# Kernel tuning notes

Measured on AMD Instinct MI355X. Metric: run time of the kernel, lower is better.

Reference implementation:

```python
import jax, jax.numpy as jnp
import numpy as np

N = 50000   # nodes
E = 400000  # edges
G = 256     # graphs in batch
D = 256     # out_dim (scalar channel width)
VD = 16     # vector channel width after v_emb


def setup_inputs() -> dict:
    key = jax.random.key(0)
    ks = jax.random.split(key, 12)

    def rn(k, shape, scale=0.02):
        return (jax.random.normal(k, shape) * scale).astype(jnp.float32)

    return dict(
        node_s=jax.random.normal(ks[0], (N, 23), jnp.float32),
        node_v=jax.random.normal(ks[1], (N, 4, 3), jnp.float32),
        edge_s=jax.random.normal(ks[2], (E, 17), jnp.float32),
        edge_index=jax.random.randint(ks[3], (2, E), 0, N, jnp.int32),
        batch=jnp.sort(jax.random.randint(ks[4], (N,), 0, G, jnp.int32)),
        Ws=rn(ks[5], (23, D)), bs=jnp.zeros((D,), jnp.float32),
        Wv=rn(ks[6], (4, VD)), bv=jnp.zeros((VD,), jnp.float32),
        We=rn(ks[7], (18, D)), be=jnp.zeros((D,), jnp.float32),
        Wm1=rn(ks[8], (2 * D + VD + D, D)), bm1=jnp.zeros((D,), jnp.float32),
        Wm2=rn(ks[9], (D, D)), bm2=jnp.zeros((D,), jnp.float32),
        Wn=rn(ks[10], (D + VD, D)), bn=jnp.zeros((D,), jnp.float32),
        gamma=jnp.ones((D,), jnp.float32), beta=jnp.zeros((D,), jnp.float32),
    )


def reference(node_s, node_v, edge_s, edge_index, batch,
              Ws, bs, Wv, bv, We, be, Wm1, bm1, Wm2, bm2, Wn, bn, gamma, beta):
    # --- embeddings ---
    s = node_s @ Ws + bs                                            # [N, D]
    e_in = jnp.concatenate([edge_s, jnp.zeros((edge_s.shape[0], 1), edge_s.dtype)], axis=-1)  # no edge_v branch
    e = e_in @ We + be                                              # [E, D]
    # v_emb: Linear over the 4 vector channels -> [N, VD, 3]
    v = jnp.einsum('nkc,ko->noc', node_v, Wv) + bv[None, :, None]
    v_norm = jnp.linalg.norm(v, axis=-1)                            # [N, VD]

    # --- SimpleGVPConv: gather -> 2-layer MLP per edge -> scatter-mean ---
    src, dst = edge_index[0], edge_index[1]                         # PyG: s_j = s[src], s_i = s[dst]
    m_in = jnp.concatenate([s[dst], s[src], v_norm[src], e], axis=-1)  # [E, 2D+VD+D]
    m = jax.nn.relu(m_in @ Wm1 + bm1) @ Wm2 + bm2                   # [E, D]
    agg = jax.ops.segment_sum(m, dst, num_segments=N)               # [N, D]
    cnt = jax.ops.segment_sum(jnp.ones((E,), m.dtype), dst, num_segments=N)
    s = s + agg / jnp.maximum(cnt, 1.0)[:, None]                    # mean aggr + residual update

    # --- node MLP: Linear -> LayerNorm -> ReLU (dropout = eval identity) ---
    feat = jnp.concatenate([s, v_norm], axis=-1)                    # [N, D+VD]
    h = feat @ Wn + bn                                              # [N, D]
    mu = h.mean(axis=-1, keepdims=True)
    var = h.var(axis=-1, keepdims=True)
    h = (h - mu) * jax.lax.rsqrt(var + 1e-5) * gamma + beta
    h = jax.nn.relu(h)

    # --- global mean pool ---
    gsum = jax.ops.segment_sum(h, batch, num_segments=G)            # [G, D]
    gcnt = jax.ops.segment_sum(jnp.ones((h.shape[0],), h.dtype), batch, num_segments=G)
    return gsum / jnp.maximum(gcnt, 1.0)[:, None]
```

## Files before the change

kernel.cpp:

```cpp
#include <hip/hip_runtime.h>
#include <hip/hip_bf16.h>

typedef unsigned short u16;
typedef __attribute__((ext_vector_type(8))) short short8;
typedef __attribute__((ext_vector_type(4))) short short4v;
typedef __attribute__((ext_vector_type(4))) float f32x4;

#define NN 50000
#define EE 400000
#define GG 256
#define MP 50048
#define KS 64
#define K2 320
#define EWS 260

static __device__ __forceinline__ __hip_bfloat16 f2b(float x) { return __float2bfloat16(x); }
static __device__ __forceinline__ float u16tof(u16 v) {
    unsigned x = ((unsigned)v) << 16;
    float f;
    __builtin_memcpy(&f, &x, 4);
    return f;
}
static __device__ __forceinline__ u16 ftou16(float x) {
    __hip_bfloat16 h = __float2bfloat16(x);
    u16 b;
    __builtin_memcpy(&b, &h, 2);
    return b;
}

static __device__ __forceinline__ float dot256(const float* __restrict__ a,
                                               const float* __restrict__ b, int c) {
    const float* __restrict__ bp = b + c;
    float s0 = 0.f, s1 = 0.f, s2 = 0.f, s3 = 0.f;
    float s4 = 0.f, s5 = 0.f, s6 = 0.f, s7 = 0.f;
#pragma unroll 4
    for (int j = 0; j < 256; j += 8) {
        s0 += a[j]     * bp[(size_t)(j)     * 256];
        s1 += a[j + 1] * bp[(size_t)(j + 1) * 256];
        s2 += a[j + 2] * bp[(size_t)(j + 2) * 256];
        s3 += a[j + 3] * bp[(size_t)(j + 3) * 256];
        s4 += a[j + 4] * bp[(size_t)(j + 4) * 256];
        s5 += a[j + 5] * bp[(size_t)(j + 5) * 256];
        s6 += a[j + 6] * bp[(size_t)(j + 6) * 256];
        s7 += a[j + 7] * bp[(size_t)(j + 7) * 256];
    }
    return ((s0 + s1) + (s2 + s3)) + ((s4 + s5) + (s6 + s7));
}

__global__ __launch_bounds__(256) void phase1(const float* __restrict__ Wm1,
                                              const float* __restrict__ Wn,
                                              const float* __restrict__ Wm2,
                                              const float* __restrict__ We,
                                              const float* __restrict__ be,
                                              const float* __restrict__ bm1,
                                              const float* __restrict__ bm2,
                                              const float* __restrict__ Ws,
                                              const float* __restrict__ bs,
                                              __hip_bfloat16* __restrict__ W1pqT,
                                              __hip_bfloat16* __restrict__ W2T,
                                              float* __restrict__ Wc, float* __restrict__ bc,
                                              float* __restrict__ crow,
                                              const float* __restrict__ node_s,
                                              const float* __restrict__ node_v,
                                              const float* __restrict__ Wv,
                                              const float* __restrict__ bv,
                                              __hip_bfloat16* __restrict__ XL2,
                                              const int* __restrict__ ei,
                                              const int* __restrict__ batch,
                                              int* __restrict__ cnt,
                                              int* __restrict__ gstart) {
    int blk = blockIdx.x, tid = threadIdx.x;
    if (blk < 64) {
        int k = blk;
#pragma unroll
        for (int half = 0; half < 2; ++half) {
            int c = half * 256 + tid;
            int cc = c & 255;
            const float* Wm1h = (c < 256) ? Wm1 : (Wm1 + 256 * 256);
            float v = 0.f;
            if (k < 23) v = dot256(&Ws[k * 256], Wm1h, cc);
            else if (k < 39) { if (c >= 256) v = Wm1[(512 + (k - 23)) * 256 + cc]; }
            else if (k == 39) v = dot256(bs, Wm1h, cc);
            W1pqT[c * KS + k] = f2b(v);
        }
    } else if (blk < 74) {
        int wb = blk - 64;
        int kt0 = (wb >> 1) * 64;
        int c0 = (wb & 1) * 128;
        int w = tid >> 6, lane = tid & 63;
        int quad = lane >> 4, l16 = lane & 15;
        f32x4 acc[4][2] = {};
        for (int jt = 0; jt < 256; jt += 32) {
            int j0 = jt + quad * 8;
            short8 af[4], bf[2];
#pragma unroll
            for (int mi = 0; mi < 4; ++mi) {
                int k = kt0 + mi * 16 + l16;
                const float* ar = nullptr;
                if (k < 23) ar = Ws + (size_t)k * 256;
                else if (k == 39) ar = bs;
                else if (k >= 40 && k < 296) ar = Wm2 + (size_t)(k - 40) * 256;
                float v0 = 0.f, v1 = 0.f, v2 = 0.f, v3 = 0.f, v4 = 0.f, v5 = 0.f, v6 = 0.f, v7 = 0.f;
                if (ar) {
                    f32x4 x0 = *(const f32x4*)(ar + j0);
                    f32x4 x1 = *(const f32x4*)(ar + j0 + 4);
                    v0 = x0[0]; v1 = x0[1]; v2 = x0[2]; v3 = x0[3];
                    v4 = x1[0]; v5 = x1[1]; v6 = x1[2]; v7 = x1[3];
                }
                af[mi][0] = (short)ftou16(v0); af[mi][1] = (short)ftou16(v1);
                af[mi][2] = (short)ftou16(v2); af[mi][3] = (short)ftou16(v3);
                af[mi][4] = (short)ftou16(v4); af[mi][5] = (short)ftou16(v5);
                af[mi][6] = (short)ftou16(v6); af[mi][7] = (short)ftou16(v7);
            }
#pragma unroll
            for (int ni = 0; ni < 2; ++ni) {
                int c = c0 + w * 32 + ni * 16 + l16;
#pragma unroll
                for (int u = 0; u < 8; ++u)
                    bf[ni][u] = (short)ftou16(Wn[(size_t)(j0 + u) * 256 + c]);
            }
#pragma unroll
            for (int mi = 0; mi < 4; ++mi) {
#pragma unroll
                for (int ni = 0; ni < 2; ++ni)
                    acc[mi][ni] = __builtin_amdgcn_mfma_f32_16x16x32_bf16(af[mi], bf[ni], acc[mi][ni], 0, 0, 0);
            }
        }
#pragma unroll
        for (int mi = 0; mi < 4; ++mi) {
#pragma unroll
            for (int ni = 0; ni < 2; ++ni) {
                int c = c0 + w * 32 + ni * 16 + l16;
#pragma unroll
                for (int r = 0; r < 4; ++r) {
                    int k = kt0 + mi * 16 + quad * 4 + r;
                    float v = acc[mi][ni][r];
                    if (k >= 23 && k < 39) v = Wn[(size_t)(256 + k - 23) * 256 + c];
                    W2T[(size_t)c * K2 + k] = f2b(v);
                }
            }
        }
    } else if (blk < 93) {
        int b = blk - 74, c = tid;
        if (b < 17) Wc[b * 256 + c] = dot256(&We[b * 256], &Wm1[528 * 256], c);
        else if (b == 17) bc[c] = bm1[c] + dot256(be, &Wm1[528 * 256], c);
        else crow[c] = dot256(bm2, Wn, c);
    } else if (blk < 12593) {
        int w = tid >> 6, lane = tid & 63;
        int n = (blk - 93) * 4 + w;
        if (n < NN) {
            float lv = (lane < 23) ? node_s[(size_t)n * 23 + lane] : 0.f;
            float vv = (lane < 12) ? node_v[(size_t)n * 12 + lane] : 0.f;
            float nvk[12];
#pragma unroll
            for (int k = 0; k < 12; ++k) nvk[k] = __shfl(vv, k, 64);
            float vn = 0.f;
            if (lane < 16) {
                float b0 = bv[lane];
                float vx = b0, vy = b0, vz = b0;
#pragma unroll
                for (int k = 0; k < 4; ++k) {
                    float wv = Wv[k * 16 + lane];
                    vx += nvk[k * 3 + 0] * wv;
                    vy += nvk[k * 3 + 1] * wv;
                    vz += nvk[k * 3 + 2] * wv;
                }
                vn = sqrtf(vx * vx + vy * vy + vz * vz);
            }
            int vsrc = (lane >= 23 && lane < 39) ? (lane - 23) : 0;
            float vbc = __shfl(vn, vsrc, 64);
            float outv;
            if (lane < 23) outv = lv;
            else if (lane < 39) outv = vbc;
            else if (lane == 39) outv = 1.f;
            else outv = 0.f;
            __hip_bfloat16* row = XL2 + (size_t)n * K2;
            row[lane] = f2b(outv);
            if (lane < 24) row[296 + lane] = f2b(0.f);
        }
    } else if (blk < 14156) {
        int e = (blk - 12593) * 256 + tid;
        if (e < EE) atomicAdd(&cnt[ei[EE + e]], 1);
    } else {
        int n = (blk - 14156) * 256 + tid;
        if (n < NN) {
            int bn = batch[n];
            int bp = (n == 0) ? -1 : batch[n - 1];
            for (int g = bp + 1; g <= bn; ++g) gstart[g] = n;
            if (n == NN - 1)
                for (int g = bn + 1; g <= GG; ++g) gstart[g] = NN;
        }
    }
}

__global__ __launch_bounds__(256) void scan1(const int* __restrict__ cnt, int* __restrict__ rowptr,
                                             int* __restrict__ bsum) {
    int tid = threadIdx.x, i = blockIdx.x * 256 + tid;
    __shared__ int sd[256];
    int v = (i < NN) ? cnt[i] : 0;
    sd[tid] = v;
    __syncthreads();
    for (int off = 1; off < 256; off <<= 1) {
        int t = (tid >= off) ? sd[tid - off] : 0;
        __syncthreads();
        sd[tid] += t;
        __syncthreads();
    }
    if (i < NN) rowptr[i] = sd[tid] - v;
    if (tid == 255) bsum[blockIdx.x] = sd[255];
}
__global__ __launch_bounds__(256) void scan2(int* __restrict__ bsum, const int* __restrict__ gstart,
                                             float* __restrict__ ginv) {
    int c = threadIdx.x;
    __shared__ int sd[256];
    int v = (c < 196) ? bsum[c] : 0;
    sd[c] = v;
    __syncthreads();
    for (int off = 1; off < 256; off <<= 1) {
        int t = (c >= off) ? sd[c - off] : 0;
        __syncthreads();
        sd[c] += t;
        __syncthreads();
    }
    if (c < 196) bsum[c] = sd[c] - v;
    ginv[c] = 1.f / fmaxf((float)(gstart[c + 1] - gstart[c]), 1.f);
}
__global__ __launch_bounds__(256) void scan3(const int* __restrict__ cnt, const int* __restrict__ bsum,
                                             int* __restrict__ rowptr, int* __restrict__ cursor) {
    int i = blockIdx.x * 256 + threadIdx.x;
    if (i < NN) {
        int v = rowptr[i] + bsum[blockIdx.x];
        rowptr[i] = v;
        cursor[i] = v;
        if (i == NN - 1) rowptr[NN] = v + cnt[i];
    }
}

__global__ __launch_bounds__(256, 2) void gemm1_fill(const u16* __restrict__ A, const u16* __restrict__ Bt,
                                                     __hip_bfloat16* __restrict__ C,
                                                     const int* __restrict__ ei, int* __restrict__ cursor,
                                                     int* __restrict__ eid, int* __restrict__ srcv,
                                                     const float* __restrict__ Wc,
                                                     u16* __restrict__ WcBf) {
    __shared__ __align__(16) u16 At[128 * 64];
    __shared__ __align__(16) u16 Bs[128 * 64];
    int blk = blockIdx.x, tid = threadIdx.x;
    if (blk >= 1564) {
        if (blk == 3127) {
            for (int idx = tid; idx < 8192; idx += 256) {
                int ni = idx >> 9;
                int l = (idx >> 3) & 63;
                int j = idx & 7;
                int k = ((l >> 4) << 3) + j;
                int c = ni * 16 + (l & 15);
                float v = (k < 17) ? Wc[k * 256 + c] : 0.f;
                WcBf[idx] = ftou16(v);
            }
            return;
        }
        int e = (blk - 1564) * 256 + tid;
        if (e < EE) {
            int d = ei[EE + e];
            int s = ei[e];
            int pos = atomicAdd(&cursor[d], 1);
            eid[pos] = e;
            srcv[pos] = s;
        }
        return;
    }
    long m0 = (long)(blk >> 2) * 128;
    long n0 = (long)(blk & 3) * 128;
    int wid = tid >> 6, lane = tid & 63;
    int wm = wid >> 1, wn = wid & 1;
    int quad = lane >> 4, l16 = lane & 15;
    f32x4 acc[4][4] = {};
    int r0 = tid >> 3;
    int cc = (tid & 7) * 8;
    const u16* Ab = A + (m0 + r0) * K2 + cc;
    const u16* Bb = Bt + (n0 + r0) * KS + cc;
#pragma unroll
    for (int i = 0; i < 4; ++i) {
        int row = r0 + i * 32;
        __builtin_amdgcn_global_load_lds(
            (const __attribute__((address_space(1))) void*)(Ab + (long)(i * 32) * K2),
            (__attribute__((address_space(3))) void*)(&At[row * 64 + cc]), 16, 0, 0);
    }
#pragma unroll
    for (int i = 0; i < 4; ++i) {
        int row = r0 + i * 32;
        __builtin_amdgcn_global_load_lds(
            (const __attribute__((address_space(1))) void*)(Bb + (long)(i * 32) * KS),
            (__attribute__((address_space(3))) void*)(&Bs[row * 64 + cc]), 16, 0, 0);
    }
    __syncthreads();
#pragma unroll
    for (int kk = 0; kk < 64; kk += 32) {
        short8 af[4], bf[4];
#pragma unroll
        for (int mi = 0; mi < 4; ++mi)
            af[mi] = *(const short8*)&At[(wm * 64 + mi * 16 + l16) * 64 + kk + quad * 8];
#pragma unroll
        for (int ni = 0; ni < 4; ++ni)
            bf[ni] = *(const short8*)&Bs[(wn * 64 + ni * 16 + l16) * 64 + kk + quad * 8];
#pragma unroll
        for (int mi = 0; mi < 4; ++mi) {
#pragma unroll
            for (int ni = 0; ni < 4; ++ni)
                acc[mi][ni] = __builtin_amdgcn_mfma_f32_16x16x32_bf16(af[mi], bf[ni], acc[mi][ni], 0, 0, 0);
        }
    }
#pragma unroll
    for (int mi = 0; mi < 4; ++mi) {
#pragma unroll
        for (int ni = 0; ni < 4; ++ni) {
            long row = m0 + wm * 64 + mi * 16 + quad * 4;
            long col = n0 + wn * 64 + ni * 16 + l16;
#pragma unroll
            for (int r = 0; r < 4; ++r)
                C[(row + r) * 512 + col] = f2b(acc[mi][ni][r]);
        }
    }
}

__global__ __launch_bounds__(64) void edge_agg(const u16* __restrict__ PQ,
                                               const float* __restrict__ edge_s,
                                               const int* __restrict__ srcv,
                                               const int* __restrict__ eid,
                                               const int* __restrict__ rowptr,
                                               const u16* __restrict__ WcBf,
                                               const float* __restrict__ bc,
                                               __hip_bfloat16* __restrict__ XL2) {
    __shared__ __align__(16) u16 EW[16 * EWS];
    int lane = threadIdx.x;
    int n = blockIdx.x;
    int start = rowptr[n], deg = rowptr[n + 1] - start;
    int l16 = lane & 15, quad = lane >> 4;
    short8 wcf[16];
#pragma unroll
    for (int ni = 0; ni < 16; ++ni)
        wcf[ni] = *(const short8*)&WcBf[ni * 512 + lane * 8];
    f32x4 bc4 = *(const f32x4*)&bc[lane * 4];
    short4v p4 = *(const short4v*)&PQ[(size_t)n * 512 + lane * 4];
    f32x4 pb;
#pragma unroll
    for (int i = 0; i < 4; ++i) pb[i] = u16tof((u16)p4[i]) + bc4[i];
    f32x4 acc = {0.f, 0.f, 0.f, 0.f};
    const f32x4 zf = {0.f, 0.f, 0.f, 0.f};
    for (int base = 0; base < deg; base += 64) {
        int m = deg - base;
        if (m > 64) m = 64;
        int mm1 = m - 1;
        int ee = 0, ss = 0;
        if (lane < m) {
            ee = eid[start + base + lane];
            ss = srcv[start + base + lane];
        }
        auto loadQ = [&](int p) {
            int pc = (p < mm1) ? p : mm1;
            int s = __builtin_amdgcn_readlane(ss, pc);
            return *(const short4v*)&PQ[(size_t)s * 512 + 256 + lane * 4];
        };
        int ng = (m + 15) >> 4;
        for (int g = 0; g < ng; ++g) {
            int b16 = g * 16;
            short4v qA0 = loadQ(b16 + 0);
            short4v qA1 = loadQ(b16 + 1);
            short4v qA2 = loadQ(b16 + 2);
            short4v qA3 = loadQ(b16 + 3);
            short4v qA4 = loadQ(b16 + 4);
            short4v qA5 = loadQ(b16 + 5);
            short4v qA6 = loadQ(b16 + 6);
            short4v qA7 = loadQ(b16 + 7);
            int li = b16 + l16;
            if (li > mm1) li = mm1;
            int ev = __shfl(ee, li, 64);
            const float* ep = edge_s + (size_t)ev * 17 + quad * 8;
            float a0 = 0.f, a1 = 0.f, a2 = 0.f, a3 = 0.f, a4 = 0.f, a5 = 0.f, a6 = 0.f, a7 = 0.f;
            if (quad < 2) {
                a0 = ep[0]; a1 = ep[1]; a2 = ep[2]; a3 = ep[3];
                a4 = ep[4]; a5 = ep[5]; a6 = ep[6]; a7 = ep[7];
            } else if (quad == 2) {
                a0 = ep[0];
            }
            short8 af;
            af[0] = (short)ftou16(a0); af[1] = (short)ftou16(a1);
            af[2] = (short)ftou16(a2); af[3] = (short)ftou16(a3);
            af[4] = (short)ftou16(a4); af[5] = (short)ftou16(a5);
            af[6] = (short)ftou16(a6); af[7] = (short)ftou16(a7);
#pragma unroll
            for (int ni = 0; ni < 16; ++ni) {
                f32x4 ew = __builtin_amdgcn_mfma_f32_16x16x32_bf16(af, wcf[ni], zf, 0, 0, 0);
#pragma unroll
                for (int r = 0; r < 4; ++r)
                    EW[(quad * 4 + r) * EWS + ni * 16 + l16] = ftou16(ew[r]);
            }
            int mg = m - b16;
            if (mg > 16) mg = 16;
            short4v qB0 = {0, 0, 0, 0}, qB1 = {0, 0, 0, 0}, qB2 = {0, 0, 0, 0}, qB3 = {0, 0, 0, 0};
            short4v qB4 = {0, 0, 0, 0}, qB5 = {0, 0, 0, 0}, qB6 = {0, 0, 0, 0}, qB7 = {0, 0, 0, 0};
            if (mg > 8) {
                qB0 = loadQ(b16 + 8);
                qB1 = loadQ(b16 + 9);
                qB2 = loadQ(b16 + 10);
                qB3 = loadQ(b16 + 11);
                qB4 = loadQ(b16 + 12);
                qB5 = loadQ(b16 + 13);
                qB6 = loadQ(b16 + 14);
                qB7 = loadQ(b16 + 15);
            }
#define CONSUME(QQ, c)                                                              \
            {                                                                       \
                int jj = (c);                                                       \
                if (jj < mg) {                                                      \
                    short4v ew4 = *(const short4v*)&EW[jj * EWS + lane * 4];        \
                    _Pragma("unroll")                                               \
                    for (int i = 0; i < 4; ++i)                                     \
                        acc[i] += fmaxf(pb[i] + u16tof((u16)QQ[i]) +                \
                                        u16tof((u16)ew4[i]), 0.f);                  \
                }                                                                   \
            }
            CONSUME(qA0, 0)  CONSUME(qA1, 1)  CONSUME(qA2, 2)  CONSUME(qA3, 3)
            CONSUME(qA4, 4)  CONSUME(qA5, 5)  CONSUME(qA6, 6)  CONSUME(qA7, 7)
            CONSUME(qB0, 8)  CONSUME(qB1, 9)  CONSUME(qB2, 10) CONSUME(qB3, 11)
            CONSUME(qB4, 12) CONSUME(qB5, 13) CONSUME(qB6, 14) CONSUME(qB7, 15)
#undef CONSUME
        }
    }
    float inv = 1.f / fmaxf((float)deg, 1.f);
    short4v ov;
#pragma unroll
    for (int i = 0; i < 4; ++i) ov[i] = (short)ftou16(acc[i] * inv);
    *(short4v*)&XL2[(size_t)n * K2 + 40 + lane * 4] = ov;
}

__global__ __launch_bounds__(256, 2) void gemm2_lnp(const u16* __restrict__ A, const u16* __restrict__ Bt,
                                                    const int* __restrict__ cnt, const int* __restrict__ batch,
                                                    const float* __restrict__ bn, const float* __restrict__ crow,
                                                    const float* __restrict__ gamma, const float* __restrict__ beta,
                                                    const float* __restrict__ ginv, float* __restrict__ out) {
    __shared__ __align__(16) u16 At[64 * 64];
    __shared__ __align__(16) u16 Bs[256 * 64];
    __shared__ float rsum[4][64], rsum2[4][64];
    __shared__ int sdeg[64], sbatch[64];
    int tid = threadIdx.x;
    long m0 = (long)blockIdx.x * 64;
    int w = tid >> 6, lane = tid & 63;
    int quad = lane >> 4, l16 = lane & 15;
    f32x4 acc[4][4] = {};
    int r0 = tid >> 3;
    int cc = (tid & 7) * 8;
    const u16* Ab = A + (m0 + r0) * K2 + cc;
    const u16* Bb = Bt + (long)r0 * K2 + cc;
    for (int kt = 0; kt < K2; kt += 64) {
#pragma unroll
        for (int i = 0; i < 2; ++i) {
            int row = r0 + i * 32;
            __builtin_amdgcn_global_load_lds(
                (const __attribute__((address_space(1))) void*)(Ab + (long)(i * 32) * K2 + kt),
                (__attribute__((address_space(3))) void*)(&At[row * 64 + cc]), 16, 0, 0);
        }
#pragma unroll
        for (int i = 0; i < 8; ++i) {
            int row = r0 + i * 32;
            __builtin_amdgcn_global_load_lds(
                (const __attribute__((address_space(1))) void*)(Bb + (long)(i * 32) * K2 + kt),
                (__attribute__((address_space(3))) void*)(&Bs[row * 64 + cc]), 16, 0, 0);
        }
        __syncthreads();
#pragma unroll
        for (int kk = 0; kk < 64; kk += 32) {
            short8 af[4], bf[4];
#pragma unroll
            for (int mi = 0; mi < 4; ++mi)
                af[mi] = *(const short8*)&At[(mi * 16 + l16) * 64 + kk + quad * 8];
#pragma unroll
            for (int ni = 0; ni < 4; ++ni)
                bf[ni] = *(const short8*)&Bs[(w * 64 + ni * 16 + l16) * 64 + kk + quad * 8];
#pragma unroll
            for (int mi = 0; mi < 4; ++mi) {
#pragma unroll
                for (int ni = 0; ni < 4; ++ni)
                    acc[mi][ni] = __builtin_amdgcn_mfma_f32_16x16x32_bf16(af[mi], bf[ni], acc[mi][ni], 0, 0, 0);
            }
        }
        __syncthreads();
    }
    if (tid < 64) {
        long n = m0 + tid;
        sdeg[tid] = (n < NN) ? cnt[n] : 0;
        sbatch[tid] = (n < NN) ? batch[n] : -1;
    }
    __syncthreads();
    float bn_l[4], cr_l[4], g_l[4], be_l[4];
#pragma unroll
    for (int ni = 0; ni < 4; ++ni) {
        int col = w * 64 + ni * 16 + l16;
        bn_l[ni] = bn[col];
        cr_l[ni] = crow[col];
        g_l[ni] = gamma[col];
        be_l[ni] = beta[col];
    }
#pragma unroll
    for (int mi = 0; mi < 4; ++mi) {
#pragma unroll
        for (int r = 0; r < 4; ++r) {
            int row = mi * 16 + quad * 4 + r;
            float cr_on = (sdeg[row] > 0) ? 1.f : 0.f;
            float s = 0.f, s2 = 0.f;
#pragma unroll
            for (int ni = 0; ni < 4; ++ni) {
                float xv = acc[mi][ni][r] + bn_l[ni] + cr_on * cr_l[ni];
                acc[mi][ni][r] = xv;
                s += xv;
                s2 += xv * xv;
            }
            s += __shfl_xor(s, 1, 64);  s2 += __shfl_xor(s2, 1, 64);
            s += __shfl_xor(s, 2, 64);  s2 += __shfl_xor(s2, 2, 64);
            s += __shfl_xor(s, 4, 64);  s2 += __shfl_xor(s2, 4, 64);
            s += __shfl_xor(s, 8, 64);  s2 += __shfl_xor(s2, 8, 64);
            if (l16 == 0) { rsum[w][row] = s; rsum2[w][row] = s2; }
        }
    }
    __syncthreads();
    float mu_a[4][4], rs_a[4][4];
#pragma unroll
    for (int mi = 0; mi < 4; ++mi) {
#pragma unroll
        for (int r = 0; r < 4; ++r) {
            int row = mi * 16 + quad * 4 + r;
            float S = rsum[0][row] + rsum[1][row] + rsum[2][row] + rsum[3][row];
            float S2 = rsum2[0][row] + rsum2[1][row] + rsum2[2][row] + rsum2[3][row];
            float mu = S * (1.f / 256.f);
            mu_a[mi][r] = mu;
            rs_a[mi][r] = rsqrtf(S2 * (1.f / 256.f) - mu * mu + 1e-5f);
        }
    }
#pragma unroll
    for (int ni = 0; ni < 4; ++ni) {
        int col = w * 64 + ni * 16 + l16;
        float pacc = 0.f;
        int curg = -1;
#pragma unroll
        for (int mi = 0; mi < 4; ++mi) {
#pragma unroll
            for (int r = 0; r < 4; ++r) {
                int row = mi * 16 + quad * 4 + r;
                int g = sbatch[row];
                float y = (acc[mi][ni][r] - mu_a[mi][r]) * rs_a[mi][r] * g_l[ni] + be_l[ni];
                y = fmaxf(y, 0.f);
                if (g != curg) {
                    if (curg >= 0) atomicAdd(&out[curg * 256 + col], pacc * ginv[curg]);
                    pacc = 0.f;
                    curg = g;
                }
                if (g >= 0) pacc += y;
            }
        }
        if (curg >= 0) atomicAdd(&out[curg * 256 + col], pacc * ginv[curg]);
    }
}

extern "C" void kernel_launch(void* const* d_in, const int* in_sizes, int n_in,
                              void* d_out, int out_size, void* d_ws, size_t ws_size,
                              hipStream_t stream) {
    const float* node_s = (const float*)d_in[0];
    const float* node_v = (const float*)d_in[1];
    const float* edge_s = (const float*)d_in[2];
    const int* ei = (const int*)d_in[3];
    const int* batch = (const int*)d_in[4];
    const float* Ws = (const float*)d_in[5];
    const float* bs = (const float*)d_in[6];
    const float* Wv = (const float*)d_in[7];
    const float* bv = (const float*)d_in[8];
    const float* We = (const float*)d_in[9];
    const float* be = (const float*)d_in[10];
    const float* Wm1 = (const float*)d_in[11];
    const float* bm1 = (const float*)d_in[12];
    const float* Wm2 = (const float*)d_in[13];
    const float* bm2 = (const float*)d_in[14];
    const float* Wn = (const float*)d_in[15];
    const float* bn = (const float*)d_in[16];
    const float* gamma = (const float*)d_in[17];
    const float* beta = (const float*)d_in[18];

    char* ws = (char*)d_ws;
    size_t off = 0;
    auto take = [&](size_t n) {
        void* p = ws + off;
        off = (off + n + 255) & ~(size_t)255;
        return p;
    };
    __hip_bfloat16* XL2 = (__hip_bfloat16*)take((size_t)MP * K2 * 2);
    __hip_bfloat16* PQ = (__hip_bfloat16*)take((size_t)MP * 512 * 2);
    __hip_bfloat16* W1pqT = (__hip_bfloat16*)take(512 * KS * 2);
    __hip_bfloat16* W2T = (__hip_bfloat16*)take(256 * K2 * 2);
    float* Wc = (float*)take(17 * 256 * 4);
    float* bc = (float*)take(256 * 4);
    float* crow = (float*)take(256 * 4);
    u16* WcBf = (u16*)take(16 * 512 * 2);
    int* cnt = (int*)take(NN * 4);
    int* gstart = (int*)take((GG + 1) * 4);
    float* ginv = (float*)take(GG * 4);
    int* rowptr = (int*)take((NN + 1) * 4);
    int* cursor = (int*)take(NN * 4);
    int* eid = (int*)take(EE * 4);
    int* srcv = (int*)take(EE * 4);
    int* bsum = (int*)take(256 * 4);

    hipMemsetAsync(cnt, 0, NN * 4, stream);
    hipMemsetAsync(d_out, 0, (size_t)out_size * 4, stream);

    phase1<<<14352, 256, 0, stream>>>(Wm1, Wn, Wm2, We, be, bm1, bm2, Ws, bs,
                                      W1pqT, W2T, Wc, bc, crow,
                                      node_s, node_v, Wv, bv, XL2, ei, batch, cnt, gstart);

    scan1<<<196, 256, 0, stream>>>(cnt, rowptr, bsum);
    scan2<<<1, 256, 0, stream>>>(bsum, gstart, ginv);
    scan3<<<196, 256, 0, stream>>>(cnt, bsum, rowptr, cursor);

    gemm1_fill<<<3128, 256, 0, stream>>>((const u16*)XL2, (const u16*)W1pqT, PQ, ei, cursor, eid,
                                         srcv, Wc, WcBf);

    edge_agg<<<NN, 64, 0, stream>>>((const u16*)PQ, edge_s, srcv, eid, rowptr, WcBf, bc, XL2);

    gemm2_lnp<<<782, 256, 0, stream>>>((const u16*)XL2, (const u16*)W2T, cnt, batch,
                                       bn, crow, gamma, beta, ginv, (float*)d_out);
}
```

Measured before the change: 291.0 us.

## Make edge_agg persistent with next-node prefetch; compute W1pq fold via MFMA

edge_agg now launches a fixed 4096 single-wave blocks that loop over nodes with stride 4096 instead of one block per node. Each block prefetches the next node's row pointers, first 64 edge/source ids and P row while it processes the current node. This amortises the per-block setup, including the 16 WcBf fragment loads, and hides index-load latency. Separately, the Ws·Wm1 fold in phase1 moves from 64 blocks of scalar dot products to 4 MFMA blocks, so fewer blocks carry more work each and load balance across nodes of different degree may suffer.

```diff
diff --git a/kernel.cpp b/kernel.cpp
--- a/kernel.cpp
+++ b/kernel.cpp
@@ -13,6 +13,7 @@
 #define KS 64
 #define K2 320
 #define EWS 260
+#define EAG 4096
 
 static __device__ __forceinline__ __hip_bfloat16 f2b(float x) { return __float2bfloat16(x); }
 static __device__ __forceinline__ float u16tof(u16 v) {
@@ -70,21 +71,65 @@
                                               int* __restrict__ cnt,
                                               int* __restrict__ gstart) {
     int blk = blockIdx.x, tid = threadIdx.x;
-    if (blk < 64) {
-        int k = blk;
-#pragma unroll
-        for (int half = 0; half < 2; ++half) {
-            int c = half * 256 + tid;
-            int cc = c & 255;
-            const float* Wm1h = (c < 256) ? Wm1 : (Wm1 + 256 * 256);
-            float v = 0.f;
-            if (k < 23) v = dot256(&Ws[k * 256], Wm1h, cc);
-            else if (k < 39) { if (c >= 256) v = Wm1[(512 + (k - 23)) * 256 + cc]; }
-            else if (k == 39) v = dot256(bs, Wm1h, cc);
-            W1pqT[c * KS + k] = f2b(v);
-        }
-    } else if (blk < 74) {
-        int wb = blk - 64;
+    if (blk < 4) {
+        int c0 = blk * 128;
+        int w = tid >> 6, lane = tid & 63;
+        int quad = lane >> 4, l16 = lane & 15;
+        f32x4 acc[4][2] = {};
+        for (int jt = 0; jt < 256; jt += 32) {
+            int j0 = jt + quad * 8;
+            short8 af[4], bf[2];
+#pragma unroll
+            for (int mi = 0; mi < 4; ++mi) {
+                int k = mi * 16 + l16;
+                const float* ar = nullptr;
+                if (k < 23) ar = Ws + (size_t)k * 256;
+                else if (k == 39) ar = bs;
+                float v0 = 0.f, v1 = 0.f, v2 = 0.f, v3 = 0.f, v4 = 0.f, v5 = 0.f, v6 = 0.f, v7 = 0.f;
+                if (ar) {
+                    f32x4 x0 = *(const f32x4*)(ar + j0);
+                    f32x4 x1 = *(const f32x4*)(ar + j0 + 4);
+                    v0 = x0[0]; v1 = x0[1]; v2 = x0[2]; v3 = x0[3];
+                    v4 = x1[0]; v5 = x1[1]; v6 = x1[2]; v7 = x1[3];
+                }
+                af[mi][0] = (short)ftou16(v0); af[mi][1] = (short)ftou16(v1);
+                af[mi][2] = (short)ftou16(v2); af[mi][3] = (short)ftou16(v3);
+                af[mi][4] = (short)ftou16(v4); af[mi][5] = (short)ftou16(v5);
+                af[mi][6] = (short)ftou16(v6); af[mi][7] = (short)ftou16(v7);
+            }
+#pragma unroll
+            for (int ni = 0; ni < 2; ++ni) {
+                int c = c0 + w * 32 + ni * 16 + l16;
+                const float* Wm1h = (c < 256) ? Wm1 : (Wm1 + 256 * 256);
+                int cc = c & 255;
+#pragma unroll
+                for (int u = 0; u < 8; ++u)
+                    bf[ni][u] = (short)ftou16(Wm1h[(size_t)(j0 + u) * 256 + cc]);
+            }
+#pragma unroll
+            for (int mi = 0; mi < 4; ++mi) {
+#pragma unroll
+                for (int ni = 0; ni < 2; ++ni)
+                    acc[mi][ni] = __builtin_amdgcn_mfma_f32_16x16x32_bf16(af[mi], bf[ni], acc[mi][ni], 0, 0, 0);
+            }
+        }
+#pragma unroll
+        for (int mi = 0; mi < 4; ++mi) {
+#pragma unroll
+            for (int ni = 0; ni < 2; ++ni) {
+                int c = c0 + w * 32 + ni * 16 + l16;
+#pragma unroll
+                for (int r = 0; r < 4; ++r) {
+                    int k = mi * 16 + quad * 4 + r;
+                    float v = acc[mi][ni][r];
+                    if (k >= 23 && k < 39)
+                        v = (c >= 256) ? Wm1[(size_t)(512 + (k - 23)) * 256 + (c & 255)] : 0.f;
+                    W1pqT[(size_t)c * KS + k] = f2b(v);
+                }
+            }
+        }
+    } else if (blk < 14) {
+        int wb = blk - 4;
         int kt0 = (wb >> 1) * 64;
         int c0 = (wb & 1) * 128;
         int w = tid >> 6, lane = tid & 63;
@@ -140,14 +185,14 @@
                 }
             }
         }
-    } else if (blk < 93) {
-        int b = blk - 74, c = tid;
+    } else if (blk < 33) {
+        int b = blk - 14, c = tid;
         if (b < 17) Wc[b * 256 + c] = dot256(&We[b * 256], &Wm1[528 * 256], c);
         else if (b == 17) bc[c] = bm1[c] + dot256(be, &Wm1[528 * 256], c);
         else crow[c] = dot256(bm2, Wn, c);
-    } else if (blk < 12593) {
+    } else if (blk < 12533) {
         int w = tid >> 6, lane = tid & 63;
-        int n = (blk - 93) * 4 + w;
+        int n = (blk - 33) * 4 + w;
         if (n < NN) {
             float lv = (lane < 23) ? node_s[(size_t)n * 23 + lane] : 0.f;
             float vv = (lane < 12) ? node_v[(size_t)n * 12 + lane] : 0.f;
@@ -178,11 +223,11 @@
             row[lane] = f2b(outv);
             if (lane < 24) row[296 + lane] = f2b(0.f);
         }
-    } else if (blk < 14156) {
-        int e = (blk - 12593) * 256 + tid;
+    } else if (blk < 14096) {
+        int e = (blk - 12533) * 256 + tid;
         if (e < EE) atomicAdd(&cnt[ei[EE + e]], 1);
     } else {
-        int n = (blk - 14156) * 256 + tid;
+        int n = (blk - 14096) * 256 + tid;
         if (n < NN) {
             int bn = batch[n];
             int bp = (n == 0) ? -1 : batch[n - 1];
@@ -332,105 +377,138 @@
                                                __hip_bfloat16* __restrict__ XL2) {
     __shared__ __align__(16) u16 EW[16 * EWS];
     int lane = threadIdx.x;
-    int n = blockIdx.x;
-    int start = rowptr[n], deg = rowptr[n + 1] - start;
     int l16 = lane & 15, quad = lane >> 4;
     short8 wcf[16];
 #pragma unroll
     for (int ni = 0; ni < 16; ++ni)
         wcf[ni] = *(const short8*)&WcBf[ni * 512 + lane * 8];
     f32x4 bc4 = *(const f32x4*)&bc[lane * 4];
+    const f32x4 zf = {0.f, 0.f, 0.f, 0.f};
+    int n = blockIdx.x;
+    int st = rowptr[n], en = rowptr[n + 1];
+    int ee = 0, ss = 0;
+    {
+        int m0 = en - st;
+        if (m0 > 64) m0 = 64;
+        if (lane < m0) {
+            ee = eid[st + lane];
+            ss = srcv[st + lane];
+        }
+    }
     short4v p4 = *(const short4v*)&PQ[(size_t)n * 512 + lane * 4];
-    f32x4 pb;
-#pragma unroll
-    for (int i = 0; i < 4; ++i) pb[i] = u16tof((u16)p4[i]) + bc4[i];
-    f32x4 acc = {0.f, 0.f, 0.f, 0.f};
-    const f32x4 zf = {0.f, 0.f, 0.f, 0.f};
-    for (int base = 0; base < deg; base += 64) {
-        int m = deg - base;
-        if (m > 64) m = 64;
-        int mm1 = m - 1;
-        int ee = 0, ss = 0;
-        if (lane < m) {
-            ee = eid[start + base + lane];
-            ss = srcv[start + base + lane];
-        }
-        auto loadQ = [&](int p) {
-            int pc = (p < mm1) ? p : mm1;
-            int s = __builtin_amdgcn_readlane(ss, pc);
-            return *(const short4v*)&PQ[(size_t)s * 512 + 256 + lane * 4];
-        };
-        int ng = (m + 15) >> 4;
-        for (int g = 0; g < ng; ++g) {
-            int b16 = g * 16;
-            short4v qA0 = loadQ(b16 + 0);
-            short4v qA1 = loadQ(b16 + 1);
-            short4v qA2 = loadQ(b16 + 2);
-            short4v qA3 = loadQ(b16 + 3);
-            short4v qA4 = loadQ(b16 + 4);
-            short4v qA5 = loadQ(b16 + 5);
-            short4v qA6 = loadQ(b16 + 6);
-            short4v qA7 = loadQ(b16 + 7);
-            int li = b16 + l16;
-            if (li > mm1) li = mm1;
-            int ev = __shfl(ee, li, 64);
-            const float* ep = edge_s + (size_t)ev * 17 + quad * 8;
-            float a0 = 0.f, a1 = 0.f, a2 = 0.f, a3 = 0.f, a4 = 0.f, a5 = 0.f, a6 = 0.f, a7 = 0.f;
-            if (quad < 2) {
-                a0 = ep[0]; a1 = ep[1]; a2 = ep[2]; a3 = ep[3];
-                a4 = ep[4]; a5 = ep[5]; a6 = ep[6]; a7 = ep[7];
-            } else if (quad == 2) {
-                a0 = ep[0];
-            }
-            short8 af;
-            af[0] = (short)ftou16(a0); af[1] = (short)ftou16(a1);
-            af[2] = (short)ftou16(a2); af[3] = (short)ftou16(a3);
-            af[4] = (short)ftou16(a4); af[5] = (short)ftou16(a5);
-            af[6] = (short)ftou16(a6); af[7] = (short)ftou16(a7);
-#pragma unroll
-            for (int ni = 0; ni < 16; ++ni) {
-                f32x4 ew = __builtin_amdgcn_mfma_f32_16x16x32_bf16(af, wcf[ni], zf, 0, 0, 0);
-#pragma unroll
-                for (int r = 0; r < 4; ++r)
-                    EW[(quad * 4 + r) * EWS + ni * 16 + l16] = ftou16(ew[r]);
-            }
-            int mg = m - b16;
-            if (mg > 16) mg = 16;
-            short4v qB0 = {0, 0, 0, 0}, qB1 = {0, 0, 0, 0}, qB2 = {0, 0, 0, 0}, qB3 = {0, 0, 0, 0};
-            short4v qB4 = {0, 0, 0, 0}, qB5 = {0, 0, 0, 0}, qB6 = {0, 0, 0, 0}, qB7 = {0, 0, 0, 0};
-            if (mg > 8) {
-                qB0 = loadQ(b16 + 8);
-                qB1 = loadQ(b16 + 9);
-                qB2 = loadQ(b16 + 10);
-                qB3 = loadQ(b16 + 11);
-                qB4 = loadQ(b16 + 12);
-                qB5 = loadQ(b16 + 13);
-                qB6 = loadQ(b16 + 14);
-                qB7 = loadQ(b16 + 15);
-            }
+    while (true) {
+        int nn = n + EAG;
+        int stN = 0, enN = 0, eeN = 0, ssN = 0;
+        short4v p4N = {0, 0, 0, 0};
+        if (nn < NN) {
+            stN = rowptr[nn];
+            enN = rowptr[nn + 1];
+            int mN = enN - stN;
+            if (mN > 64) mN = 64;
+            if (lane < mN) {
+                eeN = eid[stN + lane];
+                ssN = srcv[stN + lane];
+            }
+            p4N = *(const short4v*)&PQ[(size_t)nn * 512 + lane * 4];
+        }
+        int deg = en - st;
+        f32x4 pb;
+#pragma unroll
+        for (int i = 0; i < 4; ++i) pb[i] = u16tof((u16)p4[i]) + bc4[i];
+        f32x4 acc = {0.f, 0.f, 0.f, 0.f};
+        for (int base = 0; base < deg; base += 64) {
+            int m = deg - base;
+            if (m > 64) m = 64;
+            int mm1 = m - 1;
+            if (base > 0) {
+                ee = 0; ss = 0;
+                if (lane < m) {
+                    ee = eid[st + base + lane];
+                    ss = srcv[st + base + lane];
+                }
+            }
+            auto loadQ = [&](int p) {
+                int pc = (p < mm1) ? p : mm1;
+                int s = __builtin_amdgcn_readlane(ss, pc);
+                return *(const short4v*)&PQ[(size_t)s * 512 + 256 + lane * 4];
+            };
+            int ng = (m + 15) >> 4;
+            for (int g = 0; g < ng; ++g) {
+                int b16 = g * 16;
+                short4v qA0 = loadQ(b16 + 0);
+                short4v qA1 = loadQ(b16 + 1);
+                short4v qA2 = loadQ(b16 + 2);
+                short4v qA3 = loadQ(b16 + 3);
+                short4v qA4 = loadQ(b16 + 4);
+                short4v qA5 = loadQ(b16 + 5);
+                short4v qA6 = loadQ(b16 + 6);
+                short4v qA7 = loadQ(b16 + 7);
+                int li = b16 + l16;
+                if (li > mm1) li = mm1;
+                int ev = __shfl(ee, li, 64);
+                const float* ep = edge_s + (size_t)ev * 17 + quad * 8;
+                float a0 = 0.f, a1 = 0.f, a2 = 0.f, a3 = 0.f, a4 = 0.f, a5 = 0.f, a6 = 0.f, a7 = 0.f;
+                if (quad < 2) {
+                    a0 = ep[0]; a1 = ep[1]; a2 = ep[2]; a3 = ep[3];
+                    a4 = ep[4]; a5 = ep[5]; a6 = ep[6]; a7 = ep[7];
+                } else if (quad == 2) {
+                    a0 = ep[0];
+                }
+                short8 af;
+                af[0] = (short)ftou16(a0); af[1] = (short)ftou16(a1);
+                af[2] = (short)ftou16(a2); af[3] = (short)ftou16(a3);
+                af[4] = (short)ftou16(a4); af[5] = (short)ftou16(a5);
+                af[6] = (short)ftou16(a6); af[7] = (short)ftou16(a7);
+#pragma unroll
+                for (int ni = 0; ni < 16; ++ni) {
+                    f32x4 ew = __builtin_amdgcn_mfma_f32_16x16x32_bf16(af, wcf[ni], zf, 0, 0, 0);
+#pragma unroll
+                    for (int r = 0; r < 4; ++r)
+                        EW[(quad * 4 + r) * EWS + ni * 16 + l16] = ftou16(ew[r]);
+                }
+                int mg = m - b16;
+                if (mg > 16) mg = 16;
+                short4v qB0 = {0, 0, 0, 0}, qB1 = {0, 0, 0, 0}, qB2 = {0, 0, 0, 0}, qB3 = {0, 0, 0, 0};
+                short4v qB4 = {0, 0, 0, 0}, qB5 = {0, 0, 0, 0}, qB6 = {0, 0, 0, 0}, qB7 = {0, 0, 0, 0};
+                if (mg > 8) {
+                    qB0 = loadQ(b16 + 8);
+                    qB1 = loadQ(b16 + 9);
+                    qB2 = loadQ(b16 + 10);
+                    qB3 = loadQ(b16 + 11);
+                    qB4 = loadQ(b16 + 12);
+                    qB5 = loadQ(b16 + 13);
+                    qB6 = loadQ(b16 + 14);
+                    qB7 = loadQ(b16 + 15);
+                }
 #define CONSUME(QQ, c)                                                              \
-            {                                                                       \
-                int jj = (c);                                                       \
-                if (jj < mg) {                                                      \
-                    short4v ew4 = *(const short4v*)&EW[jj * EWS + lane * 4];        \
-                    _Pragma("unroll")                                               \
-                    for (int i = 0; i < 4; ++i)                                     \
-                        acc[i] += fmaxf(pb[i] + u16tof((u16)QQ[i]) +                \
-                                        u16tof((u16)ew4[i]), 0.f);                  \
-                }                                                                   \
-            }
-            CONSUME(qA0, 0)  CONSUME(qA1, 1)  CONSUME(qA2, 2)  CONSUME(qA3, 3)
-            CONSUME(qA4, 4)  CONSUME(qA5, 5)  CONSUME(qA6, 6)  CONSUME(qA7, 7)
-            CONSUME(qB0, 8)  CONSUME(qB1, 9)  CONSUME(qB2, 10) CONSUME(qB3, 11)
-            CONSUME(qB4, 12) CONSUME(qB5, 13) CONSUME(qB6, 14) CONSUME(qB7, 15)
+                {                                                                   \
+                    int jj = (c);                                                   \
+                    if (jj < mg) {                                                  \
+                        short4v ew4 = *(const short4v*)&EW[jj * EWS + lane * 4];    \
+                        _Pragma("unroll")                                           \
+                        for (int i = 0; i < 4; ++i)                                 \
+                            acc[i] += fmaxf(pb[i] + u16tof((u16)QQ[i]) +            \
+                                            u16tof((u16)ew4[i]), 0.f);              \
+                    }                                                               \
+                }
+                CONSUME(qA0, 0)  CONSUME(qA1, 1)  CONSUME(qA2, 2)  CONSUME(qA3, 3)
+                CONSUME(qA4, 4)  CONSUME(qA5, 5)  CONSUME(qA6, 6)  CONSUME(qA7, 7)
+                CONSUME(qB0, 8)  CONSUME(qB1, 9)  CONSUME(qB2, 10) CONSUME(qB3, 11)
+                CONSUME(qB4, 12) CONSUME(qB5, 13) CONSUME(qB6, 14) CONSUME(qB7, 15)
 #undef CONSUME
-        }
-    }
-    float inv = 1.f / fmaxf((float)deg, 1.f);
-    short4v ov;
-#pragma unroll
-    for (int i = 0; i < 4; ++i) ov[i] = (short)ftou16(acc[i] * inv);
-    *(short4v*)&XL2[(size_t)n * K2 + 40 + lane * 4] = ov;
+            }
+        }
+        float inv = 1.f / fmaxf((float)deg, 1.f);
+        short4v ov;
+#pragma unroll
+        for (int i = 0; i < 4; ++i) ov[i] = (short)ftou16(acc[i] * inv);
+        *(short4v*)&XL2[(size_t)n * K2 + 40 + lane * 4] = ov;
+        if (nn >= NN) break;
+        n = nn;
+        st = stN; en = enN;
+        ee = eeN; ss = ssN;
+        p4 = p4N;
+    }
 }
 
 __global__ __launch_bounds__(256, 2) void gemm2_lnp(const u16* __restrict__ A, const u16* __restrict__ Bt,
@@ -610,7 +688,7 @@
     hipMemsetAsync(cnt, 0, NN * 4, stream);
     hipMemsetAsync(d_out, 0, (size_t)out_size * 4, stream);
 
-    phase1<<<14352, 256, 0, stream>>>(Wm1, Wn, Wm2, We, be, bm1, bm2, Ws, bs,
+    phase1<<<14292, 256, 0, stream>>>(Wm1, Wn, Wm2, We, be, bm1, bm2, Ws, bs,
                                       W1pqT, W2T, Wc, bc, crow,
                                       node_s, node_v, Wv, bv, XL2, ei, batch, cnt, gstart);
 
@@ -621,7 +699,7 @@
     gemm1_fill<<<3128, 256, 0, stream>>>((const u16*)XL2, (const u16*)W1pqT, PQ, ei, cursor, eid,
                                          srcv, Wc, WcBf);
 
-    edge_agg<<<NN, 64, 0, stream>>>((const u16*)PQ, edge_s, srcv, eid, rowptr, WcBf, bc, XL2);
+    edge_agg<<<EAG, 64, 0, stream>>>((const u16*)PQ, edge_s, srcv, eid, rowptr, WcBf, bc, XL2);
 
     gemm2_lnp<<<782, 256, 0, stream>>>((const u16*)XL2, (const u16*)W2T, cnt, batch,
                                        bn, crow, gamma, beta, ginv, (float*)d_out);
```

Result: slower. 312.4 us (+7.4%).
